# Optimization experiments

Hardware: AMD Instinct MI355X
Metric: run time of the kernel (lower is better)

The kernel has to match this reference:

```python
import jax, jax.numpy as jnp
import numpy as np

N, B, OBS, ACT, E = 8, 8192, 128, 32, 128  # num_agents, batch, obs, act, embedding_dim


def setup_inputs() -> dict:
    key = jax.random.key(0)
    ks = jax.random.split(key, 14)
    rn = lambda k, shape: jax.random.normal(k, shape, dtype=jnp.float32) * 0.05
    return {
        'obs': jax.random.normal(ks[0], (N, B, OBS), dtype=jnp.float32),
        'act': jax.random.normal(ks[1], (N, B, ACT), dtype=jnp.float32),
        'Wg': rn(ks[2], (N, OBS + ACT, E)), 'bg': rn(ks[3], (N, E)),
        'Wq': rn(ks[4], (N, E, E)), 'bq': rn(ks[5], (N, E)),
        'Wk': rn(ks[6], (N, E, E)), 'bk': rn(ks[7], (N, E)),
        'Wv': rn(ks[8], (N, E, E)), 'bv': rn(ks[9], (N, E)),
        'W1': rn(ks[10], (N, (N + 1) * E, E)), 'b1': rn(ks[11], (N, E)),
        'W2': rn(ks[12], (N, E, 1)), 'b2': rn(ks[13], (N, 1)),
    }


def reference(obs, act, Wg, bg, Wq, bq, Wk, bk, Wv, bv, W1, b1, W2, b2):
    # per-agent embeddings e_i = relu(g_i([obs_i; act_i]))           [N,B,E]
    oa = jnp.concatenate([obs, act], axis=-1)
    e = jax.nn.relu(jnp.einsum('nbd,nde->nbe', oa, Wg) + bg[:, None, :])

    # per-(agent i, head l) queries and per-(agent j, head l) keys   [N,L,B,E]
    q = jnp.einsum('ibe,lef->ilbf', e, Wq) + bq[None, :, None, :]
    k = jnp.einsum('jbe,lef->jlbf', e, Wk) + bk[None, :, None, :]

    # scalar per-sample score key.dot(query); original applies softmax to this
    # single scalar, which is identically 1 -> softmax over a singleton axis.
    scores = jnp.einsum('ilbe,jlbe->iljb', q, k)          # [N,L,N,B]
    alpha = jax.nn.softmax(scores[..., None], axis=-1)[..., 0]  # == ones

    # values v_{l,j} = leaky_relu(V_l(e_j))                          [L,N,B,E]
    v = jax.nn.leaky_relu(jnp.einsum('jbe,lef->ljbf', e, Wv) + bv[:, None, None, :])

    # exclude j == i, aggregate: total_{i,l} = sum_{j!=i} alpha * v_{l,j}
    mask = (1.0 - jnp.eye(N, dtype=e.dtype))              # [i,j]
    w = alpha * mask[:, None, :, None]                    # [N,L,N,B]
    total = jnp.einsum('iljb,ljbe->ilbe', w, v)           # [N,L,B,E]

    # x_i = concat over heads l -> [N,B,L*E]
    xi = jnp.transpose(total, (0, 2, 1, 3)).reshape(N, B, N * E)

    # q_i = f_i([x_i; e_i])
    h = jnp.concatenate([xi, e], axis=-1)                 # [N,B,(N+1)E]
    h = jax.nn.relu(jnp.einsum('nbd,nde->nbe', h, W1) + b1[:, None, :])
    out = jnp.einsum('nbe,neo->nbo', h, W2) + b2[:, None, :]  # [N,B,1]
    return out
```

## Files before the change

kernel.cpp:

```cpp
#include <hip/hip_runtime.h>

#define DEV static __device__ __forceinline__

typedef __attribute__((ext_vector_type(8))) short short8;
typedef __attribute__((ext_vector_type(8))) __bf16 bf16x8;
typedef __attribute__((ext_vector_type(4))) float f32x4;
typedef __attribute__((ext_vector_type(2))) float f32x2;


DEV short f2bf(float f) { return __builtin_bit_cast(short, (__bf16)f); }
DEV float bf2f(short h) {
  unsigned u = ((unsigned)(unsigned short)h) << 16;
  return __builtin_bit_cast(float, u);
}
DEV f32x4 mfma16(short8 a, short8 b, f32x4 c) {
  return __builtin_amdgcn_mfma_f32_16x16x32_bf16(
      __builtin_bit_cast(bf16x8, a), __builtin_bit_cast(bf16x8, b), c, 0, 0, 0);
}
DEV void async_copy16(short* lds, const short* g) {
  __builtin_amdgcn_global_load_lds(
      (const __attribute__((address_space(1))) void*)g,
      (__attribute__((address_space(3))) void*)lds, 16, 0, 0);
}

template <int GPC, int SRC_STRIDE, int LDS_STRIDE>
DEV void stage_bt(short* lds, const short* src, int tid) {
  constexpr int TOTAL = 128 * GPC;
  #pragma unroll
  for (int g0 = 0; g0 < TOTAL; g0 += 256) {
    int g = g0 + tid;
    int c = g / GPC, kg = g % GPC;
    *(short8*)(lds + c * LDS_STRIDE + kg * 8) =
        *(const short8*)(src + c * SRC_STRIDE + kg * 8);
  }
}

__global__ __launch_bounds__(256) void k0_tr(const float* __restrict__ Wg,
                                             const float* __restrict__ Wv,
                                             const float* __restrict__ W1,
                                             short* __restrict__ WgT,
                                             short* __restrict__ WvP,
                                             short* __restrict__ W1P) {
  int g = blockIdx.x * 256 + threadIdx.x;
  short8 o;
  if (g < 20480) {
    int n = g / 2560, rem = g % 2560;
    int c = rem & 127, kg = rem >> 7;
    const float* src = Wg + n * 20480;
    #pragma unroll
    for (int j = 0; j < 8; ++j) o[j] = f2bf(src[(size_t)(kg * 8 + j) * 128 + c]);
    *(short8*)(WgT + n * 20480 + c * 160 + kg * 8) = o;
  } else if (g < 36864) {
    int g2 = g - 20480;
    int n = g2 >> 11, rem = g2 & 2047;
    int c = rem & 127, kg = rem >> 7;
    const float* src = Wv + n * 16384;
    #pragma unroll
    for (int j = 0; j < 8; ++j) o[j] = f2bf(src[(size_t)(16 * j + kg) * 128 + c]);
    *(short8*)(WvP + n * 16384 + c * 128 + kg * 8) = o;
  } else {
    int g3 = g - 36864;
    int n = g3 / 18432, rem = g3 % 18432;
    int c = rem & 127, kg = rem >> 7;
    int chunk = kg >> 4, kl = kg & 15;
    const float* src = W1 + (size_t)n * 147456;
    #pragma unroll
    for (int j = 0; j < 8; ++j)
      o[j] = f2bf(src[(size_t)(chunk * 128 + 16 * j + kl) * 128 + c]);
    *(short8*)(W1P + (size_t)n * 147456 + c * 1152 + kg * 8) = o;
  }
}

__global__ __launch_bounds__(256) void k1_e(const float* __restrict__ obs,
                                            const float* __restrict__ act,
                                            const short* __restrict__ WgT,
                                            const float* __restrict__ bg,
                                            short* __restrict__ eA) {
  __shared__ __align__(16) short BW[128 * 168];
  const int btile = blockIdx.x, n = blockIdx.y, tid = threadIdx.x;
  stage_bt<20, 160, 168>(BW, WgT + n * 20480, tid);
  __syncthreads();
  const int lane = tid & 63, wave = tid >> 6, lr = lane & 15, kg = lane >> 4;
  const int rowbase = btile * 64 + wave * 16;
  const int rowtile = btile * 4 + wave;
  f32x4 acc[8];
  #pragma unroll
  for (int m = 0; m < 8; ++m) acc[m] = f32x4{0.f, 0.f, 0.f, 0.f};
  const float* obsp = obs + (size_t)(n * 8192 + rowbase + lr) * 128;
  const float* actp = act + (size_t)(n * 8192 + rowbase + lr) * 32;
  #pragma unroll
  for (int ks = 0; ks < 5; ++ks) {
    const float* ap = (ks < 4) ? (obsp + ks * 32 + kg * 8) : (actp + kg * 8);
    float4 p0 = *(const float4*)ap;
    float4 p1 = *(const float4*)(ap + 4);
    short8 a;
    a[0] = f2bf(p0.x); a[1] = f2bf(p0.y); a[2] = f2bf(p0.z); a[3] = f2bf(p0.w);
    a[4] = f2bf(p1.x); a[5] = f2bf(p1.y); a[6] = f2bf(p1.z); a[7] = f2bf(p1.w);
    #pragma unroll
    for (int m = 0; m < 8; ++m) {
      short8 b = *(const short8*)(&BW[(m * 16 + lr) * 168 + ks * 32 + kg * 8]);
      acc[m] = mfma16(b, a, acc[m]);
    }
  }
  f32x4 bg4[8];
  #pragma unroll
  for (int m = 0; m < 8; ++m)
    bg4[m] = *(const f32x4*)(bg + n * 128 + m * 16 + kg * 4);
  #pragma unroll
  for (int r = 0; r < 4; ++r) {
    short8 pkt;
    #pragma unroll
    for (int m = 0; m < 8; ++m) {
      float x = acc[m][r] + bg4[m][r];
      pkt[m] = f2bf(x > 0.f ? x : 0.f);
    }
    *(short8*)(eA + ((size_t)(n * 512 + rowtile) * 256 + (kg * 4 + r) * 16 +
                     lr) * 8) = pkt;
  }
}

__global__ __launch_bounds__(256) void k2_V(const short* __restrict__ eA,
                                            const short* __restrict__ WvP,
                                            const float* __restrict__ bv,
                                            short* __restrict__ SBf,
                                            unsigned char* __restrict__ VBf) {
  __shared__ __align__(16) short BW[128 * 136];
  const int btile = blockIdx.x, l = blockIdx.y, tid = threadIdx.x;
  stage_bt<16, 128, 136>(BW, WvP + l * 16384, tid);
  __syncthreads();
  const int lane = tid & 63, wave = tid >> 6, lr = lane & 15, kg = lane >> 4;
  const int rowtile = btile * 4 + wave;
  f32x4 bvv4[8];
  #pragma unroll
  for (int m = 0; m < 8; ++m)
    bvv4[m] = *(const f32x4*)(bv + l * 128 + m * 16 + kg * 4);
  f32x4 Sacc[8];
  #pragma unroll
  for (int m = 0; m < 8; ++m) Sacc[m] = f32x4{0.f, 0.f, 0.f, 0.f};
  for (int j = 0; j < 8; ++j) {
    short8 a[4];
    #pragma unroll
    for (int ks = 0; ks < 4; ++ks)
      a[ks] = *(const short8*)(
          eA + ((size_t)(j * 512 + rowtile) * 256 + ks * 64 + lane) * 8);
    f32x4 acc[8];
    #pragma unroll
    for (int m = 0; m < 8; ++m) acc[m] = f32x4{0.f, 0.f, 0.f, 0.f};
    #pragma unroll
    for (int ks = 0; ks < 4; ++ks)
      #pragma unroll
      for (int m = 0; m < 8; ++m) {
        short8 b = *(const short8*)(&BW[(m * 16 + lr) * 136 + ks * 32 + kg * 8]);
        acc[m] = mfma16(b, a[ks], acc[m]);
      }
    #pragma unroll
    for (int r = 0; r < 4; ++r) {
      float x[8];
      #pragma unroll
      for (int m = 0; m < 8; ++m) {
        float t = acc[m][r] + bvv4[m][r];
        t = (t > 0.f) ? t : 0.01f * t;
        Sacc[m][r] += t;
        x[m] = t;
      }
      unsigned lo = 0, hi = 0;
      lo = __builtin_amdgcn_cvt_pk_fp8_f32(x[0], x[1], lo, false);
      lo = __builtin_amdgcn_cvt_pk_fp8_f32(x[2], x[3], lo, true);
      hi = __builtin_amdgcn_cvt_pk_fp8_f32(x[4], x[5], hi, false);
      hi = __builtin_amdgcn_cvt_pk_fp8_f32(x[6], x[7], hi, true);
      uint2 o{lo, hi};
      *(uint2*)(VBf + ((size_t)((j * 8 + l) * 512 + rowtile) * 256 +
                       (kg * 4 + r) * 16 + lr) * 8) = o;
    }
  }
  #pragma unroll
  for (int r = 0; r < 4; ++r) {
    short8 pkt;
    #pragma unroll
    for (int m = 0; m < 8; ++m) pkt[m] = f2bf(Sacc[m][r]);
    *(short8*)(SBf + ((size_t)(l * 512 + rowtile) * 256 + (kg * 4 + r) * 16 +
                      lr) * 8) = pkt;
  }
}

__global__ __launch_bounds__(256, 4) void k3_h(const short* __restrict__ eA,
                                               const short* __restrict__ SBf,
                                               const unsigned char* __restrict__ VBf,
                                               const short* __restrict__ W1P,
                                               const float* __restrict__ b1,
                                               const float* __restrict__ W2,
                                               const float* __restrict__ b2,
                                               float* __restrict__ out) {
  __shared__ __align__(16) short BW[2][128 * 64];
  const int bid = blockIdx.x;
  const int i = bid & 7;
  const int btile = bid >> 3;
  const int tid = threadIdx.x;
  const int lane = tid & 63, wave = tid >> 6, lr = lane & 15, kg = lane >> 4;
  const int lr8 = lane & 7;
  const int rowbase = btile * 64 + wave * 16;
  const int rowtile = btile * 4 + wave;
  const short* w1 = W1P + (size_t)i * 147456;

#define STAGE_W1(buf, koff)                                                    \
  {                                                                            \
    _Pragma("unroll") for (int t = 0; t < 4; ++t) {                            \
      int G = t * 256 + tid;                                                   \
      int cG = G >> 3, gl = G & 7;                                             \
      async_copy16((buf) + (t * 256 + wave * 64) * 8,                          \
                   w1 + cG * 1152 + (koff) + ((gl ^ (cG & 7)) << 3));          \
    }                                                                          \
  }

  short8 sv[2];
  uint2 vv[2];
  #pragma unroll
  for (int ks = 0; ks < 2; ++ks) {
    sv[ks] = *(const short8*)(
        SBf + ((size_t)rowtile * 256 + ks * 64 + lane) * 8);
    vv[ks] = *(const uint2*)(
        VBf + ((size_t)((i * 8) * 512 + rowtile) * 256 + ks * 64 + lane) * 8);
  }
  f32x4 hacc[8];
  #pragma unroll
  for (int m = 0; m < 8; ++m) hacc[m] = f32x4{0.f, 0.f, 0.f, 0.f};

  STAGE_W1(BW[0], 0);
  for (int c = 0; c < 18; ++c) {
    __syncthreads();
    if (c < 17) { STAGE_W1(BW[(c + 1) & 1], (c + 1) * 64); }
    short8 aa[2];
    if (c < 16) {
      #pragma unroll
      for (int ks = 0; ks < 2; ++ks) {
        f32x2 f01 = __builtin_amdgcn_cvt_pk_f32_fp8((int)vv[ks].x, false);
        f32x2 f23 = __builtin_amdgcn_cvt_pk_f32_fp8((int)vv[ks].x, true);
        f32x2 f45 = __builtin_amdgcn_cvt_pk_f32_fp8((int)vv[ks].y, false);
        f32x2 f67 = __builtin_amdgcn_cvt_pk_f32_fp8((int)vv[ks].y, true);
        aa[ks][0] = f2bf(bf2f(sv[ks][0]) - f01.x);
        aa[ks][1] = f2bf(bf2f(sv[ks][1]) - f01.y);
        aa[ks][2] = f2bf(bf2f(sv[ks][2]) - f23.x);
        aa[ks][3] = f2bf(bf2f(sv[ks][3]) - f23.y);
        aa[ks][4] = f2bf(bf2f(sv[ks][4]) - f45.x);
        aa[ks][5] = f2bf(bf2f(sv[ks][5]) - f45.y);
        aa[ks][6] = f2bf(bf2f(sv[ks][6]) - f67.x);
        aa[ks][7] = f2bf(bf2f(sv[ks][7]) - f67.y);
      }
    } else {
      aa[0] = sv[0];
      aa[1] = sv[1];
    }
    if (c + 1 < 16) {
      int l = (c + 1) >> 1, h = (c + 1) & 1;
      #pragma unroll
      for (int ks = 0; ks < 2; ++ks) {
        sv[ks] = *(const short8*)(
            SBf + (((size_t)l * 512 + rowtile) * 256 + h * 128 + ks * 64 + lane) * 8);
        vv[ks] = *(const uint2*)(
            VBf + (((size_t)(i * 8 + l) * 512 + rowtile) * 256 + h * 128 +
                   ks * 64 + lane) * 8);
      }
    } else if (c + 1 < 18) {
      int h = c + 1 - 16;
      #pragma unroll
      for (int ks = 0; ks < 2; ++ks)
        sv[ks] = *(const short8*)(
            eA + (((size_t)i * 512 + rowtile) * 256 + h * 128 + ks * 64 + lane) * 8);
    }
    const short* bw = BW[c & 1];
    #pragma unroll
    for (int ks = 0; ks < 2; ++ks)
      #pragma unroll
      for (int m = 0; m < 8; ++m) {
        short8 b = *(const short8*)(bw + (m * 16 + lr) * 64 +
                                    (((ks * 4 + kg) ^ lr8) << 3));
        hacc[m] = mfma16(aa[ks], b, hacc[m]);
      }
  }
#undef STAGE_W1

  float sacc[4] = {0.f, 0.f, 0.f, 0.f};
  #pragma unroll
  for (int m = 0; m < 8; ++m) {
    int col = m * 16 + lr;
    float b1v = b1[i * 128 + col];
    float w2v = W2[i * 128 + col];
    #pragma unroll
    for (int r = 0; r < 4; ++r) {
      float h = hacc[m][r] + b1v;
      h = h > 0.f ? h : 0.f;
      sacc[r] += h * w2v;
    }
  }
  #pragma unroll
  for (int r = 0; r < 4; ++r) {
    float v = sacc[r];
    v += __shfl_xor(v, 1);
    v += __shfl_xor(v, 2);
    v += __shfl_xor(v, 4);
    v += __shfl_xor(v, 8);
    if (lr == 0) out[i * 8192 + rowbase + kg * 4 + r] = v + b2[i];
  }
}

extern "C" void kernel_launch(void* const* d_in, const int* in_sizes, int n_in,
                              void* d_out, int out_size, void* d_ws, size_t ws_size,
                              hipStream_t stream) {
  const float* obs = (const float*)d_in[0];
  const float* act = (const float*)d_in[1];
  const float* Wg  = (const float*)d_in[2];
  const float* bg  = (const float*)d_in[3];
  const float* Wv  = (const float*)d_in[8];
  const float* bv  = (const float*)d_in[9];
  const float* W1  = (const float*)d_in[10];
  const float* b1  = (const float*)d_in[11];
  const float* W2  = (const float*)d_in[12];
  const float* b2  = (const float*)d_in[13];
  float* out = (float*)d_out;

  const size_t E_N = (size_t)8 * 8192 * 128;
  const size_t V_B = (size_t)64 * 8192 * 128;

  short* eA  = (short*)d_ws;
  unsigned char* VBf = (unsigned char*)(eA + E_N);
  short* SBf = (short*)(VBf + V_B);
  short* WgT = SBf + E_N;
  short* WvP = WgT + 163840;
  short* W1P = WvP + 131072;

  k0_tr<<<720, 256, 0, stream>>>(Wg, Wv, W1, WgT, WvP, W1P);
  k1_e<<<dim3(128, 8), 256, 0, stream>>>(obs, act, WgT, bg, eA);
  k2_V<<<dim3(128, 8), 256, 0, stream>>>(eA, WvP, bv, SBf, VBf);
  k3_h<<<1024, 256, 0, stream>>>(eA, SBf, VBf, W1P, b1, W2, b2, out);
}
```

Measured before the change: 96.41 us.

## Load W1 fragments directly from global in MFMA order; prefetch eA in k2

The W1 pre-pack kernel now writes W1 in exact per-lane MFMA fragment order, so k3 reads each B operand with one coalesced 16-byte global load. This removes the LDS double-buffering, async global-to-LDS copies and per-chunk block barriers. Separately, k2 software-prefetches the next agent's embedding rows while computing the current one. The cost is that every wave re-reads W1 from L2/global instead of sharing one LDS copy across four waves, which raises cache traffic and exposes load latency right before the MFMAs.

Result: slower. 107.2 us (+11.2%).

```diff
diff --git a/kernel.cpp b/kernel.cpp
--- a/kernel.cpp
+++ b/kernel.cpp
@@ -16,11 +16,6 @@
 DEV f32x4 mfma16(short8 a, short8 b, f32x4 c) {
   return __builtin_amdgcn_mfma_f32_16x16x32_bf16(
       __builtin_bit_cast(bf16x8, a), __builtin_bit_cast(bf16x8, b), c, 0, 0, 0);
-}
-DEV void async_copy16(short* lds, const short* g) {
-  __builtin_amdgcn_global_load_lds(
-      (const __attribute__((address_space(1))) void*)g,
-      (__attribute__((address_space(3))) void*)lds, 16, 0, 0);
 }
 
 template <int GPC, int SRC_STRIDE, int LDS_STRIDE>
@@ -40,7 +35,7 @@
                                              const float* __restrict__ W1,
                                              short* __restrict__ WgT,
                                              short* __restrict__ WvP,
-                                             short* __restrict__ W1P) {
+                                             short* __restrict__ W1B) {
   int g = blockIdx.x * 256 + threadIdx.x;
   short8 o;
   if (g < 20480) {
@@ -60,14 +55,14 @@
     *(short8*)(WvP + n * 16384 + c * 128 + kg * 8) = o;
   } else {
     int g3 = g - 36864;
-    int n = g3 / 18432, rem = g3 % 18432;
-    int c = rem & 127, kg = rem >> 7;
-    int chunk = kg >> 4, kl = kg & 15;
+    int n = g3 / 18432, G = g3 % 18432;
+    int c = G >> 10, m = (G >> 7) & 7, q = (G >> 4) & 7, lrow = G & 15;
     const float* src = W1 + (size_t)n * 147456;
+    int kbase = (c >> 1) * 128 + (c & 1) * 8 + q;
     #pragma unroll
     for (int j = 0; j < 8; ++j)
-      o[j] = f2bf(src[(size_t)(chunk * 128 + 16 * j + kl) * 128 + c]);
-    *(short8*)(W1P + (size_t)n * 147456 + c * 1152 + kg * 8) = o;
+      o[j] = f2bf(src[(size_t)(kbase + 16 * j) * 128 + m * 16 + lrow]);
+    *(short8*)(W1B + (size_t)n * 147456 + (size_t)G * 8) = o;
   }
 }
 
@@ -137,12 +132,18 @@
   f32x4 Sacc[8];
   #pragma unroll
   for (int m = 0; m < 8; ++m) Sacc[m] = f32x4{0.f, 0.f, 0.f, 0.f};
+  short8 a[4], an[4];
+  #pragma unroll
+  for (int ks = 0; ks < 4; ++ks)
+    a[ks] = *(const short8*)(
+        eA + ((size_t)rowtile * 256 + ks * 64 + lane) * 8);
   for (int j = 0; j < 8; ++j) {
-    short8 a[4];
-    #pragma unroll
-    for (int ks = 0; ks < 4; ++ks)
-      a[ks] = *(const short8*)(
-          eA + ((size_t)(j * 512 + rowtile) * 256 + ks * 64 + lane) * 8);
+    if (j + 1 < 8) {
+      #pragma unroll
+      for (int ks = 0; ks < 4; ++ks)
+        an[ks] = *(const short8*)(
+            eA + ((size_t)((j + 1) * 512 + rowtile) * 256 + ks * 64 + lane) * 8);
+    }
     f32x4 acc[8];
     #pragma unroll
     for (int m = 0; m < 8; ++m) acc[m] = f32x4{0.f, 0.f, 0.f, 0.f};
@@ -172,6 +173,8 @@
       *(uint2*)(VBf + ((size_t)((j * 8 + l) * 512 + rowtile) * 256 +
                        (kg * 4 + r) * 16 + lr) * 8) = o;
     }
+    #pragma unroll
+    for (int ks = 0; ks < 4; ++ks) a[ks] = an[ks];
   }
   #pragma unroll
   for (int r = 0; r < 4; ++r) {
@@ -186,31 +189,19 @@
 __global__ __launch_bounds__(256, 4) void k3_h(const short* __restrict__ eA,
                                                const short* __restrict__ SBf,
                                                const unsigned char* __restrict__ VBf,
-                                               const short* __restrict__ W1P,
+                                               const short* __restrict__ W1B,
                                                const float* __restrict__ b1,
                                                const float* __restrict__ W2,
                                                const float* __restrict__ b2,
                                                float* __restrict__ out) {
-  __shared__ __align__(16) short BW[2][128 * 64];
   const int bid = blockIdx.x;
   const int i = bid & 7;
   const int btile = bid >> 3;
   const int tid = threadIdx.x;
   const int lane = tid & 63, wave = tid >> 6, lr = lane & 15, kg = lane >> 4;
-  const int lr8 = lane & 7;
   const int rowbase = btile * 64 + wave * 16;
   const int rowtile = btile * 4 + wave;
-  const short* w1 = W1P + (size_t)i * 147456;
-
-#define STAGE_W1(buf, koff)                                                    \
-  {                                                                            \
-    _Pragma("unroll") for (int t = 0; t < 4; ++t) {                            \
-      int G = t * 256 + tid;                                                   \
-      int cG = G >> 3, gl = G & 7;                                             \
-      async_copy16((buf) + (t * 256 + wave * 64) * 8,                          \
-                   w1 + cG * 1152 + (koff) + ((gl ^ (cG & 7)) << 3));          \
-    }                                                                          \
-  }
+  const short* w1b = W1B + (size_t)i * 147456;
 
   short8 sv[2];
   uint2 vv[2];
@@ -225,10 +216,7 @@
   #pragma unroll
   for (int m = 0; m < 8; ++m) hacc[m] = f32x4{0.f, 0.f, 0.f, 0.f};
 
-  STAGE_W1(BW[0], 0);
   for (int c = 0; c < 18; ++c) {
-    __syncthreads();
-    if (c < 17) { STAGE_W1(BW[(c + 1) & 1], (c + 1) * 64); }
     short8 aa[2];
     if (c < 16) {
       #pragma unroll
@@ -267,17 +255,15 @@
         sv[ks] = *(const short8*)(
             eA + (((size_t)i * 512 + rowtile) * 256 + h * 128 + ks * 64 + lane) * 8);
     }
-    const short* bw = BW[c & 1];
+    const short* wb = w1b + (size_t)c * 8192;
     #pragma unroll
     for (int ks = 0; ks < 2; ++ks)
       #pragma unroll
       for (int m = 0; m < 8; ++m) {
-        short8 b = *(const short8*)(bw + (m * 16 + lr) * 64 +
-                                    (((ks * 4 + kg) ^ lr8) << 3));
+        short8 b = *(const short8*)(wb + (m * 128 + ks * 64 + lane) * 8);
         hacc[m] = mfma16(aa[ks], b, hacc[m]);
       }
   }
-#undef STAGE_W1
 
   float sacc[4] = {0.f, 0.f, 0.f, 0.f};
   #pragma unroll
@@ -326,10 +312,10 @@
   short* SBf = (short*)(VBf + V_B);
   short* WgT = SBf + E_N;
   short* WvP = WgT + 163840;
-  short* W1P = WvP + 131072;
-
-  k0_tr<<<720, 256, 0, stream>>>(Wg, Wv, W1, WgT, WvP, W1P);
+  short* W1B = WvP + 131072;
+
+  k0_tr<<<720, 256, 0, stream>>>(Wg, Wv, W1, WgT, WvP, W1B);
   k1_e<<<dim3(128, 8), 256, 0, stream>>>(obs, act, WgT, bg, eA);
   k2_V<<<dim3(128, 8), 256, 0, stream>>>(eA, WvP, bv, SBf, VBf);
-  k3_h<<<1024, 256, 0, stream>>>(eA, SBf, VBf, W1P, b1, W2, b2, out);
-}
+  k3_h<<<1024, 256, 0, stream>>>(eA, SBf, VBf, W1B, b1, W2, b2, out);
+}
```
